# Performance work log

Hardware: AMD Instinct MI355X
Metric: run time of the kernel (lower is better)

Reference implementation:

```python
import jax, jax.numpy as jnp
import numpy as np

NUM_LAYERS = 3  # min_num_layers == max_num_layers == 3 (deterministic stochastic depth)
LN_EPS = 1e-5


def setup_inputs() -> dict:
    key = jax.random.key(0)
    k1, k2, k3 = jax.random.split(key, 3)
    N, d, F = 8, 16, 512  # (batch, in_dim=out_dim, num_features)
    x = jax.random.normal(k1, (N, d, F), dtype=jnp.float32)
    W = jax.random.normal(k2, (d, F, F, d), dtype=jnp.float32)  # recurrent weight
    A = jax.random.uniform(k3, (2, F, F), dtype=jnp.float32)    # transition mats, steps 1..2
    return {"x": x, "W": W, "A": A}


def _contract(h, W, a):
    # h: (N,d,F), W: (d,F,F,o), a: (F,F) -> (N,o,F)
    # Equivalent to (h.unsqueeze(-1).unsqueeze(-1) * (W * a[...,None])).sum(1).sum(1).transpose(1,2)
    return jnp.einsum('ndf,dfgo,fg->nog', h, W, a)


def _layer_norm(y):
    # torch applies layer_norm over the channel dim (axis 1 of (N,o,F)), no affine params
    m = y.mean(axis=1, keepdims=True)
    v = y.var(axis=1, keepdims=True)
    return (y - m) / jnp.sqrt(v + LN_EPS)


def reference(x, W, A):
    history = [x]
    for i in range(1, NUM_LAYERS):
        # recurrent + residual branch: average contributions from all previous layers
        ys = [_contract(history[j], W, A[i - j - 1]) for j in range(i)]
        y = jnp.mean(jnp.stack(ys, axis=0), axis=0)
        y = _layer_norm(y)
        history.append(y)
    return history[-1]  # return_layers='last'
```

## Files before the change

kernel.cpp:

```cpp
#include <hip/hip_runtime.h>
#include <stdint.h>


#define FC   32
#define NCH  16

template <bool SECOND>
__global__ __launch_bounds__(256)
void k_contract(const float* __restrict__ W, const float* __restrict__ A,
                const float* __restrict__ in,
                float* __restrict__ p0, float* __restrict__ p1) {
    __shared__ float sx[FC][16][8];
    __shared__ float sA0[FC][16];
    __shared__ float sA1[FC][16];

    const int t  = threadIdx.x;
    const int fc = blockIdx.x;
    const int ct = blockIdx.y;
    const int f0 = fc * FC;

    if constexpr (!SECOND) {
#pragma unroll
        for (int k = 0; k < 16; ++k) {
            int idx = k * 256 + t;
            int fl = idx >> 7, d = (idx >> 3) & 15, n = idx & 7;
            sx[fl][d][n] = in[n * 8192 + d * 512 + f0 + fl];
        }
    } else {
#pragma unroll
        for (int k = 0; k < 16; ++k) {
            int idx = k * 256 + t;
            int fl = idx >> 7, o = (idx >> 3) & 15, n = idx & 7;
            float s = 0.f;
#pragma unroll
            for (int ch = 0; ch < NCH; ++ch)
                s += in[(((size_t)ch * 512 + f0 + fl) * 16 + o) * 8 + n];
            sx[fl][o][n] = s;
        }
        __syncthreads();
        {
            int fl = t >> 3, n = t & 7;
            float m = 0.f, v = 0.f;
#pragma unroll
            for (int oo = 0; oo < 16; ++oo) { float y = sx[fl][oo][n]; m += y; v += y * y; }
            m *= (1.f / 16.f);
            v = v * (1.f / 16.f) - m * m;
            float r = rsqrtf(v + 1e-5f);
#pragma unroll
            for (int oo = 0; oo < 16; ++oo) sx[fl][oo][n] = (sx[fl][oo][n] - m) * r;
        }
    }
    {
#pragma unroll
        for (int k = 0; k < 2; ++k) {
            int idx = k * 256 + t;
            int fl = idx >> 4, gl = idx & 15;
            sA0[fl][gl] = A[(size_t)(f0 + fl) * 512 + ct * 16 + gl];
            if constexpr (!SECOND)
                sA1[fl][gl] = A[262144 + (size_t)(f0 + fl) * 512 + ct * 16 + gl];
        }
    }
    __syncthreads();

    const int gl  = t >> 4;
    const int o   = t & 15;
    const int col = (ct * 16 + gl) * 16 + o;
    const float* Wc = W + col;

    float c0[8], c1[8];
#pragma unroll
    for (int n = 0; n < 8; ++n) { c0[n] = 0.f; c1[n] = 0.f; }

    for (int fl = 0; fl < FC; ++fl) {
        const int f = f0 + fl;
        float w[16];
#pragma unroll
        for (int d = 0; d < 16; ++d)
            w[d] = Wc[(size_t)d * 4194304 + (size_t)f * 8192];

        float p[8];
#pragma unroll
        for (int n = 0; n < 8; ++n) p[n] = 0.f;
#pragma unroll
        for (int d = 0; d < 16; ++d) {
            float4 xa = *reinterpret_cast<const float4*>(&sx[fl][d][0]);
            float4 xb = *reinterpret_cast<const float4*>(&sx[fl][d][4]);
            p[0] = fmaf(xa.x, w[d], p[0]);
            p[1] = fmaf(xa.y, w[d], p[1]);
            p[2] = fmaf(xa.z, w[d], p[2]);
            p[3] = fmaf(xa.w, w[d], p[3]);
            p[4] = fmaf(xb.x, w[d], p[4]);
            p[5] = fmaf(xb.y, w[d], p[5]);
            p[6] = fmaf(xb.z, w[d], p[6]);
            p[7] = fmaf(xb.w, w[d], p[7]);
        }

        const float a0 = sA0[fl][gl];
#pragma unroll
        for (int n = 0; n < 8; ++n) c0[n] = fmaf(a0, p[n], c0[n]);
        if constexpr (!SECOND) {
            const float a1 = sA1[fl][gl];
#pragma unroll
            for (int n = 0; n < 8; ++n) c1[n] = fmaf(a1, p[n], c1[n]);
        }
    }

    size_t base = ((size_t)fc * 8192 + col) * 8;
    float4* dst0 = reinterpret_cast<float4*>(p0 + base);
    dst0[0] = make_float4(c0[0], c0[1], c0[2], c0[3]);
    dst0[1] = make_float4(c0[4], c0[5], c0[6], c0[7]);
    if constexpr (!SECOND) {
        float4* dst1 = reinterpret_cast<float4*>(p1 + base);
        dst1[0] = make_float4(c1[0], c1[1], c1[2], c1[3]);
        dst1[1] = make_float4(c1[4], c1[5], c1[6], c1[7]);
    }
}

__global__ __launch_bounds__(128)
void k_final(const float* __restrict__ p1, const float* __restrict__ p2,
             float* __restrict__ out) {
    __shared__ float sh[16][8];
    int g = blockIdx.x;
    int t = threadIdx.x;
    int o = t >> 3, n = t & 7;
    float s0 = 0.f, s1 = 0.f;
#pragma unroll
    for (int ch = 0; ch < NCH; ++ch) {
        size_t idx = (((size_t)ch * 512 + g) * 16 + o) * 8 + n;
        s0 += p1[idx];
        s1 += p2[idx];
    }
    float s = 0.5f * (s0 + s1);
    sh[o][n] = s;
    __syncthreads();
    float m = 0.f, v = 0.f;
#pragma unroll
    for (int oo = 0; oo < 16; ++oo) { float y = sh[oo][n]; m += y; v += y * y; }
    m *= (1.f / 16.f);
    v = v * (1.f / 16.f) - m * m;
    float r = rsqrtf(v + 1e-5f);
    out[n * 8192 + o * 512 + g] = (s - m) * r;
}

extern "C" void kernel_launch(void* const* d_in, const int* in_sizes, int n_in,
                              void* d_out, int out_size, void* d_ws, size_t ws_size,
                              hipStream_t stream) {
    const float* x = (const float*)d_in[0];
    const float* W = (const float*)d_in[1];
    const float* A = (const float*)d_in[2];
    float* out = (float*)d_out;

    float* ws  = (float*)d_ws;
    float* c0p = ws;
    float* c1p = c0p + 1048576;
    float* c2p = c1p + 1048576;

    k_contract<false><<<dim3(NCH, 32), 256, 0, stream>>>(W, A, x,   c0p, c1p);
    k_contract<true ><<<dim3(NCH, 32), 256, 0, stream>>>(W, A, c0p, c2p, nullptr);
    k_final<<<512, 128, 0, stream>>>(c1p, c2p, out);
}
```

Before: 412.9 us.

## Write fp16 re-laid-out weight copy in first pass, read it in second

```diff
diff --git a/kernel.cpp b/kernel.cpp
--- a/kernel.cpp
+++ b/kernel.cpp
@@ -5,11 +5,13 @@
 #define FC   32
 #define NCH  16
 
-template <bool SECOND>
+typedef _Float16 h8 __attribute__((ext_vector_type(8)));
+
 __global__ __launch_bounds__(256)
-void k_contract(const float* __restrict__ W, const float* __restrict__ A,
-                const float* __restrict__ in,
-                float* __restrict__ p0, float* __restrict__ p1) {
+void k_pass_a(const float* __restrict__ W, const float* __restrict__ A,
+              const float* __restrict__ x,
+              float* __restrict__ p0, float* __restrict__ p1,
+              _Float16* __restrict__ Wh) {
     __shared__ float sx[FC][16][8];
     __shared__ float sA0[FC][16];
     __shared__ float sA1[FC][16];
@@ -19,46 +21,18 @@
     const int ct = blockIdx.y;
     const int f0 = fc * FC;
 
-    if constexpr (!SECOND) {
-#pragma unroll
-        for (int k = 0; k < 16; ++k) {
-            int idx = k * 256 + t;
-            int fl = idx >> 7, d = (idx >> 3) & 15, n = idx & 7;
-            sx[fl][d][n] = in[n * 8192 + d * 512 + f0 + fl];
-        }
-    } else {
-#pragma unroll
-        for (int k = 0; k < 16; ++k) {
-            int idx = k * 256 + t;
-            int fl = idx >> 7, o = (idx >> 3) & 15, n = idx & 7;
-            float s = 0.f;
-#pragma unroll
-            for (int ch = 0; ch < NCH; ++ch)
-                s += in[(((size_t)ch * 512 + f0 + fl) * 16 + o) * 8 + n];
-            sx[fl][o][n] = s;
-        }
-        __syncthreads();
-        {
-            int fl = t >> 3, n = t & 7;
-            float m = 0.f, v = 0.f;
-#pragma unroll
-            for (int oo = 0; oo < 16; ++oo) { float y = sx[fl][oo][n]; m += y; v += y * y; }
-            m *= (1.f / 16.f);
-            v = v * (1.f / 16.f) - m * m;
-            float r = rsqrtf(v + 1e-5f);
-#pragma unroll
-            for (int oo = 0; oo < 16; ++oo) sx[fl][oo][n] = (sx[fl][oo][n] - m) * r;
-        }
-    }
-    {
-#pragma unroll
-        for (int k = 0; k < 2; ++k) {
-            int idx = k * 256 + t;
-            int fl = idx >> 4, gl = idx & 15;
-            sA0[fl][gl] = A[(size_t)(f0 + fl) * 512 + ct * 16 + gl];
-            if constexpr (!SECOND)
-                sA1[fl][gl] = A[262144 + (size_t)(f0 + fl) * 512 + ct * 16 + gl];
-        }
+#pragma unroll
+    for (int k = 0; k < 16; ++k) {
+        int idx = k * 256 + t;
+        int fl = idx >> 7, d = (idx >> 3) & 15, n = idx & 7;
+        sx[fl][d][n] = x[n * 8192 + d * 512 + f0 + fl];
+    }
+#pragma unroll
+    for (int k = 0; k < 2; ++k) {
+        int idx = k * 256 + t;
+        int fl = idx >> 4, gl = idx & 15;
+        sA0[fl][gl] = A[(size_t)(f0 + fl) * 512 + ct * 16 + gl];
+        sA1[fl][gl] = A[262144 + (size_t)(f0 + fl) * 512 + ct * 16 + gl];
     }
     __syncthreads();
 
@@ -77,6 +51,15 @@
 #pragma unroll
         for (int d = 0; d < 16; ++d)
             w[d] = Wc[(size_t)d * 4194304 + (size_t)f * 8192];
+
+        {
+            h8 lo, hi;
+#pragma unroll
+            for (int d = 0; d < 8; ++d) { lo[d] = (_Float16)w[d]; hi[d] = (_Float16)w[d + 8]; }
+            h8* wp = reinterpret_cast<h8*>(Wh + ((size_t)f * 8192 + col) * 16);
+            wp[0] = lo;
+            wp[1] = hi;
+        }
 
         float p[8];
 #pragma unroll
@@ -96,12 +79,11 @@
         }
 
         const float a0 = sA0[fl][gl];
-#pragma unroll
-        for (int n = 0; n < 8; ++n) c0[n] = fmaf(a0, p[n], c0[n]);
-        if constexpr (!SECOND) {
-            const float a1 = sA1[fl][gl];
-#pragma unroll
-            for (int n = 0; n < 8; ++n) c1[n] = fmaf(a1, p[n], c1[n]);
+        const float a1 = sA1[fl][gl];
+#pragma unroll
+        for (int n = 0; n < 8; ++n) {
+            c0[n] = fmaf(a0, p[n], c0[n]);
+            c1[n] = fmaf(a1, p[n], c1[n]);
         }
     }
 
@@ -109,11 +91,94 @@
     float4* dst0 = reinterpret_cast<float4*>(p0 + base);
     dst0[0] = make_float4(c0[0], c0[1], c0[2], c0[3]);
     dst0[1] = make_float4(c0[4], c0[5], c0[6], c0[7]);
-    if constexpr (!SECOND) {
-        float4* dst1 = reinterpret_cast<float4*>(p1 + base);
-        dst1[0] = make_float4(c1[0], c1[1], c1[2], c1[3]);
-        dst1[1] = make_float4(c1[4], c1[5], c1[6], c1[7]);
-    }
+    float4* dst1 = reinterpret_cast<float4*>(p1 + base);
+    dst1[0] = make_float4(c1[0], c1[1], c1[2], c1[3]);
+    dst1[1] = make_float4(c1[4], c1[5], c1[6], c1[7]);
+}
+
+__global__ __launch_bounds__(256)
+void k_pass_b(const _Float16* __restrict__ Wh, const float* __restrict__ A,
+              const float* __restrict__ c0p, float* __restrict__ p2) {
+    __shared__ float sx[FC][16][8];
+    __shared__ float sA0[FC][16];
+
+    const int t  = threadIdx.x;
+    const int fc = blockIdx.x;
+    const int ct = blockIdx.y;
+    const int f0 = fc * FC;
+
+#pragma unroll
+    for (int k = 0; k < 16; ++k) {
+        int idx = k * 256 + t;
+        int fl = idx >> 7, o = (idx >> 3) & 15, n = idx & 7;
+        float s = 0.f;
+#pragma unroll
+        for (int ch = 0; ch < NCH; ++ch)
+            s += c0p[(((size_t)ch * 512 + f0 + fl) * 16 + o) * 8 + n];
+        sx[fl][o][n] = s;
+    }
+    __syncthreads();
+    {
+        int fl = t >> 3, n = t & 7;
+        float m = 0.f, v = 0.f;
+#pragma unroll
+        for (int oo = 0; oo < 16; ++oo) { float y = sx[fl][oo][n]; m += y; v += y * y; }
+        m *= (1.f / 16.f);
+        v = v * (1.f / 16.f) - m * m;
+        float r = rsqrtf(v + 1e-5f);
+#pragma unroll
+        for (int oo = 0; oo < 16; ++oo) sx[fl][oo][n] = (sx[fl][oo][n] - m) * r;
+    }
+#pragma unroll
+    for (int k = 0; k < 2; ++k) {
+        int idx = k * 256 + t;
+        int fl = idx >> 4, gl = idx & 15;
+        sA0[fl][gl] = A[(size_t)(f0 + fl) * 512 + ct * 16 + gl];
+    }
+    __syncthreads();
+
+    const int gl  = t >> 4;
+    const int col = ct * 256 + t;
+
+    float c2[8];
+#pragma unroll
+    for (int n = 0; n < 8; ++n) c2[n] = 0.f;
+
+    for (int fl = 0; fl < FC; ++fl) {
+        const int f = f0 + fl;
+        const h8* wp = reinterpret_cast<const h8*>(Wh + ((size_t)f * 8192 + col) * 16);
+        h8 lo = wp[0];
+        h8 hi = wp[1];
+        float w[16];
+#pragma unroll
+        for (int d = 0; d < 8; ++d) { w[d] = (float)lo[d]; w[d + 8] = (float)hi[d]; }
+
+        float p[8];
+#pragma unroll
+        for (int n = 0; n < 8; ++n) p[n] = 0.f;
+#pragma unroll
+        for (int d = 0; d < 16; ++d) {
+            float4 xa = *reinterpret_cast<const float4*>(&sx[fl][d][0]);
+            float4 xb = *reinterpret_cast<const float4*>(&sx[fl][d][4]);
+            p[0] = fmaf(xa.x, w[d], p[0]);
+            p[1] = fmaf(xa.y, w[d], p[1]);
+            p[2] = fmaf(xa.z, w[d], p[2]);
+            p[3] = fmaf(xa.w, w[d], p[3]);
+            p[4] = fmaf(xb.x, w[d], p[4]);
+            p[5] = fmaf(xb.y, w[d], p[5]);
+            p[6] = fmaf(xb.z, w[d], p[6]);
+            p[7] = fmaf(xb.w, w[d], p[7]);
+        }
+
+        const float a0 = sA0[fl][gl];
+#pragma unroll
+        for (int n = 0; n < 8; ++n) c2[n] = fmaf(a0, p[n], c2[n]);
+    }
+
+    size_t base = ((size_t)fc * 8192 + col) * 8;
+    float4* dst = reinterpret_cast<float4*>(p2 + base);
+    dst[0] = make_float4(c2[0], c2[1], c2[2], c2[3]);
+    dst[1] = make_float4(c2[4], c2[5], c2[6], c2[7]);
 }
 
 __global__ __launch_bounds__(128)
@@ -154,8 +219,9 @@
     float* c0p = ws;
     float* c1p = c0p + 1048576;
     float* c2p = c1p + 1048576;
-
-    k_contract<false><<<dim3(NCH, 32), 256, 0, stream>>>(W, A, x,   c0p, c1p);
-    k_contract<true ><<<dim3(NCH, 32), 256, 0, stream>>>(W, A, c0p, c2p, nullptr);
+    _Float16* Wh = (_Float16*)(c2p + 1048576);
+
+    k_pass_a<<<dim3(NCH, 32), 256, 0, stream>>>(W, A, x, c0p, c1p, Wh);
+    k_pass_b<<<dim3(NCH, 32), 256, 0, stream>>>(Wh, A, c0p, c2p);
     k_final<<<512, 128, 0, stream>>>(c1p, c2p, out);
 }
```

New measurement: 422.7 us. 2.4% more time.

## Double the f-chunk split, prefetch next W slice, reverse order in second pass

Applied to the files above, without the earlier changes.

```diff
diff --git a/kernel.cpp b/kernel.cpp
--- a/kernel.cpp
+++ b/kernel.cpp
@@ -2,8 +2,8 @@
 #include <stdint.h>
 
 
-#define FC   32
-#define NCH  16
+#define FC   16
+#define NCH  32
 
 template <bool SECOND>
 __global__ __launch_bounds__(256)
@@ -21,24 +21,28 @@
 
     if constexpr (!SECOND) {
 #pragma unroll
-        for (int k = 0; k < 16; ++k) {
+        for (int k = 0; k < 8; ++k) {
             int idx = k * 256 + t;
             int fl = idx >> 7, d = (idx >> 3) & 15, n = idx & 7;
             sx[fl][d][n] = in[n * 8192 + d * 512 + f0 + fl];
         }
     } else {
 #pragma unroll
-        for (int k = 0; k < 16; ++k) {
+        for (int k = 0; k < 8; ++k) {
             int idx = k * 256 + t;
             int fl = idx >> 7, o = (idx >> 3) & 15, n = idx & 7;
-            float s = 0.f;
+            float s0 = 0.f, s1 = 0.f, s2 = 0.f, s3 = 0.f;
 #pragma unroll
-            for (int ch = 0; ch < NCH; ++ch)
-                s += in[(((size_t)ch * 512 + f0 + fl) * 16 + o) * 8 + n];
-            sx[fl][o][n] = s;
+            for (int ch = 0; ch < NCH; ch += 4) {
+                s0 += in[(((size_t)(ch + 0) * 512 + f0 + fl) * 16 + o) * 8 + n];
+                s1 += in[(((size_t)(ch + 1) * 512 + f0 + fl) * 16 + o) * 8 + n];
+                s2 += in[(((size_t)(ch + 2) * 512 + f0 + fl) * 16 + o) * 8 + n];
+                s3 += in[(((size_t)(ch + 3) * 512 + f0 + fl) * 16 + o) * 8 + n];
+            }
+            sx[fl][o][n] = (s0 + s1) + (s2 + s3);
         }
         __syncthreads();
-        {
+        if (t < 128) {
             int fl = t >> 3, n = t & 7;
             float m = 0.f, v = 0.f;
 #pragma unroll
@@ -51,32 +55,39 @@
         }
     }
     {
-#pragma unroll
-        for (int k = 0; k < 2; ++k) {
-            int idx = k * 256 + t;
-            int fl = idx >> 4, gl = idx & 15;
-            sA0[fl][gl] = A[(size_t)(f0 + fl) * 512 + ct * 16 + gl];
-            if constexpr (!SECOND)
-                sA1[fl][gl] = A[262144 + (size_t)(f0 + fl) * 512 + ct * 16 + gl];
-        }
+        int fl = t >> 4, gl = t & 15;
+        sA0[fl][gl] = A[(size_t)(f0 + fl) * 512 + ct * 16 + gl];
+        if constexpr (!SECOND)
+            sA1[fl][gl] = A[262144 + (size_t)(f0 + fl) * 512 + ct * 16 + gl];
     }
     __syncthreads();
 
     const int gl  = t >> 4;
-    const int o   = t & 15;
-    const int col = (ct * 16 + gl) * 16 + o;
+    const int col = ct * 256 + t;
     const float* Wc = W + col;
 
     float c0[8], c1[8];
 #pragma unroll
     for (int n = 0; n < 8; ++n) { c0[n] = 0.f; c1[n] = 0.f; }
 
-    for (int fl = 0; fl < FC; ++fl) {
-        const int f = f0 + fl;
-        float w[16];
+    float w[16], wn[16];
+    auto FL = [&](int s) { return SECOND ? (FC - 1 - s) : s; };
+    {
+        const int f = f0 + FL(0);
 #pragma unroll
         for (int d = 0; d < 16; ++d)
             w[d] = Wc[(size_t)d * 4194304 + (size_t)f * 8192];
+    }
+
+#pragma unroll
+    for (int s = 0; s < FC; ++s) {
+        const int fl = FL(s);
+        if (s + 1 < FC) {
+            const int fnext = f0 + FL(s + 1);
+#pragma unroll
+            for (int d = 0; d < 16; ++d)
+                wn[d] = Wc[(size_t)d * 4194304 + (size_t)fnext * 8192];
+        }
 
         float p[8];
 #pragma unroll
@@ -103,6 +114,11 @@
 #pragma unroll
             for (int n = 0; n < 8; ++n) c1[n] = fmaf(a1, p[n], c1[n]);
         }
+
+        if (s + 1 < FC) {
+#pragma unroll
+            for (int d = 0; d < 16; ++d) w[d] = wn[d];
+        }
     }
 
     size_t base = ((size_t)fc * 8192 + col) * 8;
@@ -123,14 +139,15 @@
     int g = blockIdx.x;
     int t = threadIdx.x;
     int o = t >> 3, n = t & 7;
-    float s0 = 0.f, s1 = 0.f;
+    float s0 = 0.f, s1 = 0.f, s2 = 0.f, s3 = 0.f;
 #pragma unroll
-    for (int ch = 0; ch < NCH; ++ch) {
-        size_t idx = (((size_t)ch * 512 + g) * 16 + o) * 8 + n;
-        s0 += p1[idx];
-        s1 += p2[idx];
+    for (int ch = 0; ch < NCH; ch += 2) {
+        size_t i0 = (((size_t)(ch + 0) * 512 + g) * 16 + o) * 8 + n;
+        size_t i1 = (((size_t)(ch + 1) * 512 + g) * 16 + o) * 8 + n;
+        s0 += p1[i0]; s1 += p2[i0];
+        s2 += p1[i1]; s3 += p2[i1];
     }
-    float s = 0.5f * (s0 + s1);
+    float s = 0.5f * ((s0 + s1) + (s2 + s3));
     sh[o][n] = s;
     __syncthreads();
     float m = 0.f, v = 0.f;
@@ -152,8 +169,8 @@
 
     float* ws  = (float*)d_ws;
     float* c0p = ws;
-    float* c1p = c0p + 1048576;
-    float* c2p = c1p + 1048576;
+    float* c1p = c0p + 2097152;
+    float* c2p = c1p + 2097152;
 
     k_contract<false><<<dim3(NCH, 32), 256, 0, stream>>>(W, A, x,   c0p, c1p);
     k_contract<true ><<<dim3(NCH, 32), 256, 0, stream>>>(W, A, c0p, c2p, nullptr);
```

New measurement: 456.3 us. +10.5%, slower.

## Double-buffer W tiles into LDS via async global_load_lds with reversed order in second pass

Applied to the files above, without the earlier changes.

```diff
diff --git a/kernel.cpp b/kernel.cpp
--- a/kernel.cpp
+++ b/kernel.cpp
@@ -4,6 +4,13 @@
 
 #define FC   32
 #define NCH  16
+
+typedef const __attribute__((address_space(1))) uint32_t* gp1_t;
+typedef __attribute__((address_space(3))) uint32_t* lp3_t;
+
+__device__ __forceinline__ void gl_lds16(const void* g, void* l) {
+    __builtin_amdgcn_global_load_lds((gp1_t)g, (lp3_t)l, 16, 0, 0);
+}
 
 template <bool SECOND>
 __global__ __launch_bounds__(256)
@@ -13,6 +20,7 @@
     __shared__ float sx[FC][16][8];
     __shared__ float sA0[FC][16];
     __shared__ float sA1[FC][16];
+    __shared__ float wbuf[2][4][16][64];
 
     const int t  = threadIdx.x;
     const int fc = blockIdx.x;
@@ -50,49 +58,66 @@
             for (int oo = 0; oo < 16; ++oo) sx[fl][oo][n] = (sx[fl][oo][n] - m) * r;
         }
     }
-    {
 #pragma unroll
-        for (int k = 0; k < 2; ++k) {
-            int idx = k * 256 + t;
-            int fl = idx >> 4, gl = idx & 15;
-            sA0[fl][gl] = A[(size_t)(f0 + fl) * 512 + ct * 16 + gl];
-            if constexpr (!SECOND)
-                sA1[fl][gl] = A[262144 + (size_t)(f0 + fl) * 512 + ct * 16 + gl];
-        }
+    for (int k = 0; k < 2; ++k) {
+        int idx = k * 256 + t;
+        int fl = idx >> 4, gl = idx & 15;
+        sA0[fl][gl] = A[(size_t)(f0 + fl) * 512 + ct * 16 + gl];
+        if constexpr (!SECOND)
+            sA1[fl][gl] = A[262144 + (size_t)(f0 + fl) * 512 + ct * 16 + gl];
     }
     __syncthreads();
 
-    const int gl  = t >> 4;
-    const int o   = t & 15;
-    const int col = (ct * 16 + gl) * 16 + o;
-    const float* Wc = W + col;
+    const int w  = t >> 6;
+    const int l  = t & 63;
+    const int gl = t >> 4;
+    const int colbase = ct * 256 + w * 64;
+    const int col = colbase + l;
+
+    auto FL = [&](int s) { return SECOND ? (FC - 1 - s) : s; };
+
+    auto stage = [&](int s, int b) {
+        const int f = f0 + FL(s);
+#pragma unroll
+        for (int k = 0; k < 4; ++k) {
+            const float* g = W + (size_t)(4 * k + (l >> 4)) * 4194304
+                               + (size_t)f * 8192 + colbase + (l & 15) * 4;
+            gl_lds16(g, &wbuf[b][w][4 * k][0]);
+        }
+    };
 
     float c0[8], c1[8];
 #pragma unroll
     for (int n = 0; n < 8; ++n) { c0[n] = 0.f; c1[n] = 0.f; }
 
-    for (int fl = 0; fl < FC; ++fl) {
-        const int f = f0 + fl;
-        float w[16];
-#pragma unroll
-        for (int d = 0; d < 16; ++d)
-            w[d] = Wc[(size_t)d * 4194304 + (size_t)f * 8192];
+    stage(0, 0);
+    stage(1, 1);
+
+#pragma unroll 2
+    for (int s = 0; s < FC; ++s) {
+        const int fl  = FL(s);
+        const int cur = s & 1;
+
+        if (s + 1 < FC) asm volatile("s_waitcnt vmcnt(4)" ::: "memory");
+        else            asm volatile("s_waitcnt vmcnt(0)" ::: "memory");
+        __builtin_amdgcn_sched_barrier(0);
 
         float p[8];
 #pragma unroll
         for (int n = 0; n < 8; ++n) p[n] = 0.f;
 #pragma unroll
         for (int d = 0; d < 16; ++d) {
+            float wd  = wbuf[cur][w][d][l];
             float4 xa = *reinterpret_cast<const float4*>(&sx[fl][d][0]);
             float4 xb = *reinterpret_cast<const float4*>(&sx[fl][d][4]);
-            p[0] = fmaf(xa.x, w[d], p[0]);
-            p[1] = fmaf(xa.y, w[d], p[1]);
-            p[2] = fmaf(xa.z, w[d], p[2]);
-            p[3] = fmaf(xa.w, w[d], p[3]);
-            p[4] = fmaf(xb.x, w[d], p[4]);
-            p[5] = fmaf(xb.y, w[d], p[5]);
-            p[6] = fmaf(xb.z, w[d], p[6]);
-            p[7] = fmaf(xb.w, w[d], p[7]);
+            p[0] = fmaf(xa.x, wd, p[0]);
+            p[1] = fmaf(xa.y, wd, p[1]);
+            p[2] = fmaf(xa.z, wd, p[2]);
+            p[3] = fmaf(xa.w, wd, p[3]);
+            p[4] = fmaf(xb.x, wd, p[4]);
+            p[5] = fmaf(xb.y, wd, p[5]);
+            p[6] = fmaf(xb.z, wd, p[6]);
+            p[7] = fmaf(xb.w, wd, p[7]);
         }
 
         const float a0 = sA0[fl][gl];
@@ -102,6 +127,11 @@
             const float a1 = sA1[fl][gl];
 #pragma unroll
             for (int n = 0; n < 8; ++n) c1[n] = fmaf(a1, p[n], c1[n]);
+        }
+
+        if (s + 2 < FC) {
+            __builtin_amdgcn_sched_barrier(0);
+            stage(s + 2, cur);
         }
     }
 
```

Measured after the change: 414.6 us. No clear change (+0.4%).
